# Kernel optimization log

Measured on AMD Instinct MI355X. Metric: run time of the kernel, lower is better.

## Reference

```python
import jax, jax.numpy as jnp
import numpy as np

N_PER = 128   # nodes per graph
G = 256       # graphs in batch
DEG = 4       # out-degree per node
IN = 768
H = 256
R = 4         # num_relations
C = 4         # num classes
RATIO = 0.25
N = G * N_PER
E_G = N_PER * DEG
E = G * E_G
K = int(np.ceil(RATIO * E_G))  # edges kept per graph by sparse_topk


def _build_edges():
    # per graph: edges (i, (i+o) mod n) for o in 1..DEG; offsets < n/2 so the
    # symmetrized edge set has no duplicate pairs (torch.unique is a no-op)
    i = np.arange(N_PER)
    src_l = np.concatenate([i for _ in range(DEG)])
    dst_l = np.concatenate([(i + o) % N_PER for o in range(1, DEG + 1)])
    offs = np.repeat(np.arange(G) * N_PER, E_G)
    src = np.tile(src_l, G) + offs
    dst = np.tile(dst_l, G) + offs
    return jnp.asarray(np.stack([src, dst]), dtype=jnp.int32)


def setup_inputs() -> dict:
    key = jax.random.key(0)
    ks = jax.random.split(key, 20)
    s = 0.02
    inp = {
        'x': jax.random.normal(ks[0], (N, IN), jnp.float32),
        'edge_index': _build_edges(),
        'edge_type': jax.random.randint(ks[1], (E,), 0, R, jnp.int32),
        'y': jax.random.randint(ks[2], (G,), 0, C, jnp.int32),
        # Generator
        'gen_w': jax.random.normal(ks[3], (IN, H), jnp.float32) * s,
        'gen_b': jnp.zeros((H,), jnp.float32),
        'att_w1': jax.random.normal(ks[4], (2 * H, 4 * H), jnp.float32) * s,
        'att_b1': jnp.zeros((4 * H,), jnp.float32),
        'att_w2': jax.random.normal(ks[5], (4 * H, 1), jnp.float32) * s,
        'att_b2': jnp.zeros((1,), jnp.float32),
        # RGCNEncoder
        'in_w': jax.random.normal(ks[6], (IN, H), jnp.float32) * s,
        'in_b': jnp.zeros((H,), jnp.float32),
        'rel_w': jax.random.normal(ks[7], (2, R, H, H), jnp.float32) * s,
        'root_w': jax.random.normal(ks[8], (2, H, H), jnp.float32) * s,
        'conv_b': jnp.zeros((2, H), jnp.float32),
        # classifier head
        'cls_w1': jax.random.normal(ks[9], (2 * H, H), jnp.float32) * s,
        'cls_b1': jnp.zeros((H,), jnp.float32),
        'cls_w2': jax.random.normal(ks[10], (H, C), jnp.float32) * s,
        'cls_b2': jnp.zeros((C,), jnp.float32),
    }
    return inp


def _rgcn_encode(x, ei, et, in_w, in_b, rel_w, root_w, conv_b):
    # linear_in + LeakyReLU
    h = jax.nn.leaky_relu(x @ in_w + in_b)
    src, dst = ei[0], ei[1]
    for l in range(2):  # two RGCNConv layers (dropout is identity in eval)
        out = h @ root_w[l] + conv_b[l]
        for r in range(R):  # per-relation gather-transform-scatter, mean aggr
            m = (et == r)
            xw = h @ rel_w[l, r]                            # [N,H]
            msg = jnp.where(m[:, None], xw[src], 0.0)       # [E,H]
            agg = jax.ops.segment_sum(msg, dst, num_segments=N)
            deg = jax.ops.segment_sum(m.astype(h.dtype), dst, num_segments=N)
            out = out + agg / jnp.maximum(deg, 1.0)[:, None]
        h = out
    ptr = jnp.arange(G) * N_PER  # data.ptr[:-1]: first node of each graph
    return h[ptr]                # [G,H]


def reference(x, edge_index, edge_type, y, gen_w, gen_b, att_w1, att_b1,
              att_w2, att_b2, in_w, in_b, rel_w, root_w, conv_b,
              cls_w1, cls_b1, cls_w2, cls_b2):
    src, dst = edge_index[0], edge_index[1]

    # ----- initial representation on the full graph -----
    initial_rep = _rgcn_encode(x, edge_index, edge_type,
                               in_w, in_b, rel_w, root_w, conv_b)

    # ----- Generator: edge scores -----
    hg = jax.nn.leaky_relu(x @ gen_w + gen_b)
    edge_rep = jnp.concatenate([hg[src], hg[dst]], axis=-1)      # [E,2H]
    score = (jax.nn.relu(edge_rep @ att_w1 + att_b1) @ att_w2 + att_b2)
    score = score.reshape(-1)                                    # [E]

    # ----- split_graph: per-graph top-k (ratio=0.25, descending) -----
    # edges are grouped contiguously per graph with E_G edges each
    sg = score.reshape(G, E_G)
    _, idx = jax.lax.top_k(sg, K)                                # [G,K]
    kept = (idx + (jnp.arange(G) * E_G)[:, None]).reshape(-1)    # global ids

    # ----- graph_sample: keep + symmetrize (unique is a no-op here) -----
    ks_, kd_, kt_ = src[kept], dst[kept], edge_type[kept]
    ei2 = jnp.stack([jnp.concatenate([ks_, kd_]),
                     jnp.concatenate([kd_, ks_])])               # [2, 2*G*K]
    et2 = jnp.concatenate([kt_, kt_])

    learned_rep = _rgcn_encode(x, ei2, et2,
                               in_w, in_b, rel_w, root_w, conv_b)

    # ----- classifier + cross entropy -----
    rep = jnp.concatenate([initial_rep, learned_rep], axis=-1)   # [G,2H]
    logits = jax.nn.leaky_relu(rep @ cls_w1 + cls_b1) @ cls_w2 + cls_b2
    logp = jax.nn.log_softmax(logits, axis=-1)
    loss = -jnp.mean(logp[jnp.arange(G), y])
    return (logits, loss, y)
```

## Files before the change

### kernel.cpp

```cpp
#include <hip/hip_runtime.h>
#include <hip/hip_bf16.h>

typedef __bf16 bf16_t;
typedef __bf16 bf16x8 __attribute__((ext_vector_type(8)));
typedef __bf16 bf16x4 __attribute__((ext_vector_type(4)));
typedef float  f32x4  __attribute__((ext_vector_type(4)));

#define NNODES 32768
#define NPER   128
#define NGRAPH 256
#define NEDGE  131072
#define EPERG  512
#define KKEEP  128
#define M1     5376
#define PLANE1 (M1 * 256)

__global__ void prep_kernel(const float* __restrict__ in_w,
                            const float* __restrict__ gen_w,
                            const float* __restrict__ att_w1,
                            const float* __restrict__ rel_w,
                            const float* __restrict__ root_w,
                            const float* __restrict__ in_b,
                            const float* __restrict__ gen_b,
                            bf16_t* __restrict__ wbf,
                            bf16_t* __restrict__ attT,
                            bf16_t* __restrict__ lw,
                            float*  __restrict__ biasws)
{
  int idx = blockIdx.x * 256 + threadIdx.x;
  if (idx < 393216) {
    int which = idx / 196608, rem = idx % 196608;
    int n = rem / 768, k = rem % 768;
    const float* w = which ? gen_w : in_w;
    wbf[idx] = (bf16_t)w[k * 256 + n];
  } else if (idx < 917504) {
    int i2 = idx - 393216;
    int half = i2 / 262144, rem = i2 % 262144;
    int n = rem / 256, k = rem % 256;
    attT[i2] = (bf16_t)att_w1[(half * 256 + k) * 1024 + n];
  } else if (idx < 1572864) {
    int i3 = idx - 917504;
    int l = i3 / 327680, rem = i3 % 327680;
    int z = rem / 65536, r2 = rem % 65536;
    int n = r2 / 256, k = r2 % 256;
    float v = (z == 0) ? root_w[(l * 256 + k) * 256 + n]
                       : rel_w[((l * 4 + (z - 1)) * 256 + k) * 256 + n];
    lw[i3] = (bf16_t)v;
  } else if (idx < 1573376) {
    int j = idx - 1572864;
    biasws[j] = (j < 256) ? in_b[j] : gen_b[j - 256];
  }
}

__global__ void cast_x_kernel(const float* __restrict__ x, bf16_t* __restrict__ xb)
{
  long i = (long)blockIdx.x * 256 + threadIdx.x;
  const float4* xf = (const float4*)x;
  float4 a = xf[i * 2], b = xf[i * 2 + 1];
  bf16x8 v;
  v[0] = (bf16_t)a.x; v[1] = (bf16_t)a.y; v[2] = (bf16_t)a.z; v[3] = (bf16_t)a.w;
  v[4] = (bf16_t)b.x; v[5] = (bf16_t)b.y; v[6] = (bf16_t)b.z; v[7] = (bf16_t)b.w;
  ((bf16x8*)xb)[i] = v;
}

template<int ACT, bool HAS_BIAS, typename OUT_T>
__global__ __launch_bounds__(512, 1) void gemm_bt2(
    const bf16_t* __restrict__ A, const bf16_t* __restrict__ BT,
    const float* __restrict__ bias, OUT_T* __restrict__ C,
    int M, int K, int colShift, long slabStride)
{
  __shared__ bf16_t sA[8192];
  __shared__ bf16_t sB[16384];
  const int tid = threadIdx.x;
  const int lane = tid & 63, wid = tid >> 6;
  const int wr = wid >> 2, wc = wid & 3;
  const long row0 = (long)blockIdx.x * 128;
  const long n0  = (long)blockIdx.y * 256;

  f32x4 acc[4][4];
  #pragma unroll
  for (int m = 0; m < 4; ++m)
    #pragma unroll
    for (int n = 0; n < 4; ++n)
      #pragma unroll
      for (int j = 0; j < 4; ++j) acc[m][n][j] = 0.f;

  for (int kt = 0; kt < K; kt += 64) {
    #pragma unroll
    for (int p = 0; p < 2; ++p) {
      const int P = p * 8192 + tid * 16;
      const int row = P >> 7;
      const int cch = ((P >> 4) & 7) ^ (row & 7);
      const bf16_t* ga = A + (row0 + row) * (long)K + kt + cch * 8;
      bf16_t* la = sA + p * 4096 + wid * 512;
      __builtin_amdgcn_global_load_lds((__attribute__((address_space(1))) void*)ga,
                                       (__attribute__((address_space(3))) void*)la, 16, 0, 0);
    }
    #pragma unroll
    for (int q = 0; q < 4; ++q) {
      const int P = q * 8192 + tid * 16;
      const int row = P >> 7;
      const int cch = ((P >> 4) & 7) ^ (row & 7);
      const bf16_t* gb = BT + (n0 + row) * (long)K + kt + cch * 8;
      bf16_t* lb = sB + q * 4096 + wid * 512;
      __builtin_amdgcn_global_load_lds((__attribute__((address_space(1))) void*)gb,
                                       (__attribute__((address_space(3))) void*)lb, 16, 0, 0);
    }
    __syncthreads();
    const char* cA = (const char*)sA;
    const char* cB = (const char*)sB;
    #pragma unroll
    for (int kk = 0; kk < 2; ++kk) {
      bf16x8 af[4], bfr[4];
      #pragma unroll
      for (int m = 0; m < 4; ++m) {
        const int row = wr * 64 + m * 16 + (lane & 15);
        const int inb = (((lane >> 4) * 16) + kk * 64) ^ ((row & 7) << 4);
        af[m] = *(const bf16x8*)(cA + row * 128 + inb);
      }
      #pragma unroll
      for (int n = 0; n < 4; ++n) {
        const int row = wc * 64 + n * 16 + (lane & 15);
        const int inb = (((lane >> 4) * 16) + kk * 64) ^ ((row & 7) << 4);
        bfr[n] = *(const bf16x8*)(cB + row * 128 + inb);
      }
      #pragma unroll
      for (int m = 0; m < 4; ++m)
        #pragma unroll
        for (int n = 0; n < 4; ++n)
          acc[m][n] = __builtin_amdgcn_mfma_f32_16x16x32_bf16(af[m], bfr[n], acc[m][n], 0, 0, 0);
    }
    __syncthreads();
  }
  const int ncolsM1 = (1 << colShift) - 1;
  #pragma unroll
  for (int n = 0; n < 4; ++n) {
    const int col = (int)n0 + wc * 64 + n * 16 + (lane & 15);
    const int slab = col >> colShift;
    const int cin = col & ncolsM1;
    float bv = 0.f;
    if (HAS_BIAS) bv = bias[col];
    #pragma unroll
    for (int m = 0; m < 4; ++m) {
      #pragma unroll
      for (int j = 0; j < 4; ++j) {
        const long row = row0 + wr * 64 + m * 16 + (lane >> 4) * 4 + j;
        float v = acc[m][n][j] + bv;
        if (ACT == 1) v = (v > 0.f) ? v : 0.01f * v;
        C[(long)slab * slabStride + (row << colShift) + cin] = (OUT_T)v;
      }
    }
  }
}

__global__ void score_kernel(const bf16_t* __restrict__ Abuf, const bf16_t* __restrict__ Bbuf,
                             const int* __restrict__ src, const int* __restrict__ dst,
                             const float* __restrict__ b1, const float* __restrict__ w2,
                             const float* __restrict__ b2, float* __restrict__ scores)
{
  __shared__ float sb1[1024], sw2[1024];
  for (int i = threadIdx.x; i < 1024; i += 256) { sb1[i] = b1[i]; sw2[i] = w2[i]; }
  __syncthreads();
  const int wid = threadIdx.x >> 6, lane = threadIdx.x & 63;
  const int e = blockIdx.x * 4 + wid;
  const int s = src[e], d = dst[e];
  const bf16x8* ar = (const bf16x8*)(Abuf + (long)s * 1024);
  const bf16x8* br = (const bf16x8*)(Bbuf + (long)d * 1024);
  float acc = 0.f;
  #pragma unroll
  for (int half = 0; half < 2; ++half) {
    bf16x8 av = ar[lane * 2 + half];
    bf16x8 bv = br[lane * 2 + half];
    const int jb = (lane * 2 + half) * 8;
    #pragma unroll
    for (int j = 0; j < 8; ++j) {
      float v = (float)av[j] + (float)bv[j] + sb1[jb + j];
      v = v > 0.f ? v : 0.f;
      acc += v * sw2[jb + j];
    }
  }
  #pragma unroll
  for (int off = 32; off > 0; off >>= 1) acc += __shfl_down(acc, off);
  if (lane == 0) scores[e] = acc + b2[0];
}

__global__ void topk_kernel(const float* __restrict__ scores,
                            const int* __restrict__ src, const int* __restrict__ dst,
                            const int* __restrict__ et,
                            int* __restrict__ ksrc, int* __restrict__ kdst, int* __restrict__ ktyp)
{
  const int g = blockIdx.x;
  __shared__ float sc[512];
  __shared__ int   id[512];
  for (int i = threadIdx.x; i < 512; i += 256) { sc[i] = scores[g * 512 + i]; id[i] = i; }
  for (int k2 = 2; k2 <= 512; k2 <<= 1) {
    for (int j = k2 >> 1; j > 0; j >>= 1) {
      __syncthreads();
      for (int t = threadIdx.x; t < 512; t += 256) {
        const int p = t ^ j;
        if (p > t) {
          float s1 = sc[t], s2 = sc[p];
          int   i1 = id[t], i2 = id[p];
          bool kgt = (s1 < s2) || (s1 == s2 && i1 > i2);
          bool up  = ((t & k2) == 0);
          if (kgt == up) { sc[t] = s2; sc[p] = s1; id[t] = i2; id[p] = i1; }
        }
      }
    }
  }
  __syncthreads();
  if (threadIdx.x < 128) {
    const int e = g * 512 + id[threadIdx.x];
    const int o = g * 128 + threadIdx.x;
    ksrc[o] = src[e]; kdst[o] = dst[e]; ktyp[o] = et[e];
  }
}

__global__ void csr_count(const int* __restrict__ ksrc, const int* __restrict__ kdst,
                          int* __restrict__ counts)
{
  const int i = blockIdx.x * 256 + threadIdx.x;
  if (i >= NGRAPH * KKEEP) return;
  atomicAdd(&counts[kdst[i]], 1);
  atomicAdd(&counts[ksrc[i]], 1);
}

__global__ void csr_offsets(const int* __restrict__ counts, int* __restrict__ offs,
                            int* __restrict__ cursor)
{
  const int g = blockIdx.x, t = threadIdx.x;
  __shared__ int s[128];
  const int mc = counts[g * 128 + t];
  s[t] = mc;
  __syncthreads();
  for (int dd = 1; dd < 128; dd <<= 1) {
    int v = (t >= dd) ? s[t - dd] : 0;
    __syncthreads();
    s[t] += v;
    __syncthreads();
  }
  const int o = g * 256 + (s[t] - mc);
  offs[g * 128 + t] = o;
  cursor[g * 128 + t] = o;
}

__global__ void csr_fill(const int* __restrict__ ksrc, const int* __restrict__ kdst,
                         const int* __restrict__ ktyp, int* __restrict__ cursor,
                         int* __restrict__ nsrc, int* __restrict__ ntyp)
{
  const int i = blockIdx.x * 256 + threadIdx.x;
  if (i >= NGRAPH * KKEEP) return;
  const int s = ksrc[i], d = kdst[i], t = ktyp[i];
  int p = atomicAdd(&cursor[d], 1); nsrc[p] = s; ntyp[p] = t;
  int q = atomicAdd(&cursor[s], 1); nsrc[q] = d; ntyp[q] = t;
}


__global__ void agg_struct_sel(const bf16_t* __restrict__ xw0, const int* __restrict__ et,
                               const float* __restrict__ conv_b, bf16_t* __restrict__ h1g)
{
  const int wid = threadIdx.x >> 6, lane = threadIdx.x & 63;
  const int row = blockIdx.x * 4 + wid;
  const int g = row / 5, slot = row % 5;
  const int d = (slot == 0) ? 0 : (128 - slot);
  const int n = g * 128 + d;
  const int c = lane * 4;
  int rt[4], si[4];
  #pragma unroll
  for (int oo = 0; oo < 4; ++oo) {
    const int i = (d - oo - 1 + 128) & 127;
    rt[oo] = et[g * 512 + oo * 128 + i];
    si[oo] = g * 128 + i;
  }
  const float4 cb = *(const float4*)(conv_b + c);
  bf16x4 rv = *(const bf16x4*)(xw0 + (long)n * 256 + c);
  float acc[4] = { (float)rv[0] + cb.x, (float)rv[1] + cb.y,
                   (float)rv[2] + cb.z, (float)rv[3] + cb.w };
  float s0[4] = {0,0,0,0}, s1[4] = {0,0,0,0}, s2[4] = {0,0,0,0}, s3[4] = {0,0,0,0};
  int d0 = 0, d1 = 0, d2 = 0, d3 = 0;
  #pragma unroll
  for (int oo = 0; oo < 4; ++oo) {
    const int t = rt[oo];
    bf16x4 w = *(const bf16x4*)(xw0 + ((long)(t + 1) * NNODES + si[oo]) * 256 + c);
    if (t == 0)      { d0++; for (int j = 0; j < 4; ++j) s0[j] += (float)w[j]; }
    else if (t == 1) { d1++; for (int j = 0; j < 4; ++j) s1[j] += (float)w[j]; }
    else if (t == 2) { d2++; for (int j = 0; j < 4; ++j) s2[j] += (float)w[j]; }
    else             { d3++; for (int j = 0; j < 4; ++j) s3[j] += (float)w[j]; }
  }
  if (d0) { float r = 1.f / d0; for (int j = 0; j < 4; ++j) acc[j] += s0[j] * r; }
  if (d1) { float r = 1.f / d1; for (int j = 0; j < 4; ++j) acc[j] += s1[j] * r; }
  if (d2) { float r = 1.f / d2; for (int j = 0; j < 4; ++j) acc[j] += s2[j] * r; }
  if (d3) { float r = 1.f / d3; for (int j = 0; j < 4; ++j) acc[j] += s3[j] * r; }
  bf16x4 ov; for (int j = 0; j < 4; ++j) ov[j] = (bf16_t)acc[j];
  *(bf16x4*)(h1g + (long)row * 256 + c) = ov;
}

__global__ void agg_csr_sel(const bf16_t* __restrict__ xw0, const int* __restrict__ offs,
                            const int* __restrict__ cnts, const int* __restrict__ nsrc,
                            const int* __restrict__ ntyp, const float* __restrict__ conv_b,
                            bf16_t* __restrict__ h1g)
{
  const int wid = threadIdx.x >> 6, lane = threadIdx.x & 63;
  const int idx = blockIdx.x * 4 + wid;
  const int g = idx >> 4, slot = idx & 15;
  const int off0 = offs[g * 128], cnt0 = cnts[g * 128];
  if (slot > cnt0) return;
  const int v = (slot == 0) ? g * 128 : nsrc[off0 + slot - 1];
  const int row = 1280 + idx;
  const int offv = offs[v], cntv = cnts[v];
  const int c = lane * 4;
  const float4 cb = *(const float4*)(conv_b + c);
  bf16x4 rv = *(const bf16x4*)(xw0 + (long)v * 256 + c);
  float acc[4] = { (float)rv[0] + cb.x, (float)rv[1] + cb.y,
                   (float)rv[2] + cb.z, (float)rv[3] + cb.w };
  float s0[4] = {0,0,0,0}, s1[4] = {0,0,0,0}, s2[4] = {0,0,0,0}, s3[4] = {0,0,0,0};
  int d0 = 0, d1 = 0, d2 = 0, d3 = 0;
  for (int j = 0; j < cntv; ++j) {
    const int t = ntyp[offv + j];
    const int sv = nsrc[offv + j];
    bf16x4 w = *(const bf16x4*)(xw0 + ((long)(t + 1) * NNODES + sv) * 256 + c);
    if (t == 0)      { d0++; for (int q = 0; q < 4; ++q) s0[q] += (float)w[q]; }
    else if (t == 1) { d1++; for (int q = 0; q < 4; ++q) s1[q] += (float)w[q]; }
    else if (t == 2) { d2++; for (int q = 0; q < 4; ++q) s2[q] += (float)w[q]; }
    else             { d3++; for (int q = 0; q < 4; ++q) s3[q] += (float)w[q]; }
  }
  if (d0) { float r = 1.f / d0; for (int q = 0; q < 4; ++q) acc[q] += s0[q] * r; }
  if (d1) { float r = 1.f / d1; for (int q = 0; q < 4; ++q) acc[q] += s1[q] * r; }
  if (d2) { float r = 1.f / d2; for (int q = 0; q < 4; ++q) acc[q] += s2[q] * r; }
  if (d3) { float r = 1.f / d3; for (int q = 0; q < 4; ++q) acc[q] += s3[q] * r; }
  bf16x4 ov; for (int q = 0; q < 4; ++q) ov[q] = (bf16_t)acc[q];
  *(bf16x4*)(h1g + (long)row * 256 + c) = ov;
}

__global__ void fagg_init(const bf16_t* __restrict__ xw1, const int* __restrict__ et,
                          const float* __restrict__ conv_b1, float* __restrict__ h2I)
{
  const int wid = threadIdx.x >> 6, lane = threadIdx.x & 63;
  const int g = blockIdx.x * 4 + wid;
  const int base = g * 5;
  const int c = lane * 4;
  const float4 cb = *(const float4*)(conv_b1 + c);
  bf16x4 rv = *(const bf16x4*)(xw1 + (long)base * 256 + c);
  float acc[4] = { (float)rv[0] + cb.x, (float)rv[1] + cb.y,
                   (float)rv[2] + cb.z, (float)rv[3] + cb.w };
  float s0[4] = {0,0,0,0}, s1[4] = {0,0,0,0}, s2[4] = {0,0,0,0}, s3[4] = {0,0,0,0};
  int d0 = 0, d1 = 0, d2 = 0, d3 = 0;
  #pragma unroll
  for (int o = 1; o <= 4; ++o) {
    const int t = et[g * 512 + (o - 1) * 128 + (128 - o)];
    bf16x4 w = *(const bf16x4*)(xw1 + ((long)(t + 1) * M1 + base + o) * 256 + c);
    if (t == 0)      { d0++; for (int q = 0; q < 4; ++q) s0[q] += (float)w[q]; }
    else if (t == 1) { d1++; for (int q = 0; q < 4; ++q) s1[q] += (float)w[q]; }
    else if (t == 2) { d2++; for (int q = 0; q < 4; ++q) s2[q] += (float)w[q]; }
    else             { d3++; for (int q = 0; q < 4; ++q) s3[q] += (float)w[q]; }
  }
  if (d0) { float r = 1.f / d0; for (int q = 0; q < 4; ++q) acc[q] += s0[q] * r; }
  if (d1) { float r = 1.f / d1; for (int q = 0; q < 4; ++q) acc[q] += s1[q] * r; }
  if (d2) { float r = 1.f / d2; for (int q = 0; q < 4; ++q) acc[q] += s2[q] * r; }
  if (d3) { float r = 1.f / d3; for (int q = 0; q < 4; ++q) acc[q] += s3[q] * r; }
  *(float4*)(h2I + (long)g * 256 + c) = make_float4(acc[0], acc[1], acc[2], acc[3]);
}

__global__ void fagg_learn(const bf16_t* __restrict__ xw1, const int* __restrict__ offs,
                           const int* __restrict__ cnts, const int* __restrict__ ntyp,
                           const float* __restrict__ conv_b1, float* __restrict__ h2L)
{
  const int wid = threadIdx.x >> 6, lane = threadIdx.x & 63;
  const int g = blockIdx.x * 4 + wid;
  const int base = 1280 + g * 16;
  const int off0 = offs[g * 128], cnt0 = cnts[g * 128];
  const int c = lane * 4;
  const float4 cb = *(const float4*)(conv_b1 + c);
  bf16x4 rv = *(const bf16x4*)(xw1 + (long)base * 256 + c);
  float acc[4] = { (float)rv[0] + cb.x, (float)rv[1] + cb.y,
                   (float)rv[2] + cb.z, (float)rv[3] + cb.w };
  float s0[4] = {0,0,0,0}, s1[4] = {0,0,0,0}, s2[4] = {0,0,0,0}, s3[4] = {0,0,0,0};
  int d0 = 0, d1 = 0, d2 = 0, d3 = 0;
  for (int j = 0; j < cnt0; ++j) {
    const int t = ntyp[off0 + j];
    bf16x4 w = *(const bf16x4*)(xw1 + ((long)(t + 1) * M1 + base + 1 + j) * 256 + c);
    if (t == 0)      { d0++; for (int q = 0; q < 4; ++q) s0[q] += (float)w[q]; }
    else if (t == 1) { d1++; for (int q = 0; q < 4; ++q) s1[q] += (float)w[q]; }
    else if (t == 2) { d2++; for (int q = 0; q < 4; ++q) s2[q] += (float)w[q]; }
    else             { d3++; for (int q = 0; q < 4; ++q) s3[q] += (float)w[q]; }
  }
  if (d0) { float r = 1.f / d0; for (int q = 0; q < 4; ++q) acc[q] += s0[q] * r; }
  if (d1) { float r = 1.f / d1; for (int q = 0; q < 4; ++q) acc[q] += s1[q] * r; }
  if (d2) { float r = 1.f / d2; for (int q = 0; q < 4; ++q) acc[q] += s2[q] * r; }
  if (d3) { float r = 1.f / d3; for (int q = 0; q < 4; ++q) acc[q] += s3[q] * r; }
  *(float4*)(h2L + (long)g * 256 + c) = make_float4(acc[0], acc[1], acc[2], acc[3]);
}

__global__ void classifier_kernel(const float* __restrict__ h2I, const float* __restrict__ h2L,
                                  const float* __restrict__ w1, const float* __restrict__ b1,
                                  const float* __restrict__ w2, const float* __restrict__ b2,
                                  const int* __restrict__ y, float* __restrict__ out,
                                  float* __restrict__ logp)
{
  const int g = blockIdx.x, t = threadIdx.x;
  __shared__ float rep[512];
  __shared__ float hid[256];
  __shared__ float lg[4];
  rep[t] = h2I[g * 256 + t];
  rep[256 + t] = h2L[g * 256 + t];
  __syncthreads();
  float a = b1[t];
  for (int i = 0; i < 512; ++i) a += rep[i] * w1[i * 256 + t];
  hid[t] = a > 0.f ? a : 0.01f * a;
  __syncthreads();
  if (t < 4) {
    float s = b2[t];
    for (int j = 0; j < 256; ++j) s += hid[j] * w2[j * 4 + t];
    lg[t] = s;
    out[g * 4 + t] = s;
  }
  __syncthreads();
  if (t == 0) {
    float m = fmaxf(fmaxf(lg[0], lg[1]), fmaxf(lg[2], lg[3]));
    float se = expf(lg[0] - m) + expf(lg[1] - m) + expf(lg[2] - m) + expf(lg[3] - m);
    logp[g] = lg[y[g]] - (m + logf(se));
  }
}

__global__ void finalize_kernel(const float* __restrict__ logp, const int* __restrict__ y,
                                float* __restrict__ out)
{
  __shared__ float s[256];
  const int t = threadIdx.x;
  s[t] = logp[t];
  __syncthreads();
  for (int d = 128; d > 0; d >>= 1) {
    if (t < d) s[t] += s[t + d];
    __syncthreads();
  }
  if (t == 0) out[1024] = -s[0] / 256.f;
  out[1025 + t] = (float)y[t];
}

extern "C" void kernel_launch(void* const* d_in, const int* in_sizes, int n_in,
                              void* d_out, int out_size, void* d_ws, size_t ws_size,
                              hipStream_t stream)
{
  (void)in_sizes; (void)n_in; (void)out_size; (void)ws_size;
  const float* x      = (const float*)d_in[0];
  const int*   ei     = (const int*)d_in[1];
  const int*   et     = (const int*)d_in[2];
  const int*   y      = (const int*)d_in[3];
  const float* gen_w  = (const float*)d_in[4];
  const float* gen_b  = (const float*)d_in[5];
  const float* att_w1 = (const float*)d_in[6];
  const float* att_b1 = (const float*)d_in[7];
  const float* att_w2 = (const float*)d_in[8];
  const float* att_b2 = (const float*)d_in[9];
  const float* in_w   = (const float*)d_in[10];
  const float* in_b   = (const float*)d_in[11];
  const float* rel_w  = (const float*)d_in[12];
  const float* root_w = (const float*)d_in[13];
  const float* conv_b = (const float*)d_in[14];
  const float* cls_w1 = (const float*)d_in[15];
  const float* cls_b1 = (const float*)d_in[16];
  const float* cls_w2 = (const float*)d_in[17];
  const float* cls_b2 = (const float*)d_in[18];
  const int* src = ei;
  const int* dst = ei + NEDGE;

  char* ws = (char*)d_ws;
  size_t off = 134217728;
  const size_t oBIG = 0;
  auto alloc = [&](size_t bytes) { size_t r = off; off += (bytes + 255) & ~(size_t)255; return r; };
  const size_t oH0  = alloc((size_t)NNODES * 256 * 2);
  const size_t oHG  = alloc((size_t)NNODES * 256 * 2);
  const size_t oH1G = alloc((size_t)M1 * 256 * 2);
  const size_t oXW1 = alloc((size_t)5 * M1 * 256 * 2);
  const size_t oSC  = alloc((size_t)NEDGE * 4);
  const size_t oKS  = alloc((size_t)NGRAPH * KKEEP * 4);
  const size_t oKD  = alloc((size_t)NGRAPH * KKEEP * 4);
  const size_t oKT  = alloc((size_t)NGRAPH * KKEEP * 4);
  const size_t oCNT = alloc((size_t)NNODES * 4);
  const size_t oOFF = alloc((size_t)NNODES * 4);
  const size_t oCUR = alloc((size_t)NNODES * 4);
  const size_t oNS  = alloc((size_t)2 * NGRAPH * KKEEP * 4);
  const size_t oNT  = alloc((size_t)2 * NGRAPH * KKEEP * 4);
  const size_t oWBF = alloc((size_t)2 * 256 * 768 * 2);
  const size_t oATT = alloc((size_t)2 * 1024 * 256 * 2);
  const size_t oLW  = alloc((size_t)2 * 5 * 256 * 256 * 2);
  const size_t oBIA = alloc(512 * 4);
  const size_t oH2I = alloc((size_t)NGRAPH * 256 * 4);
  const size_t oH2L = alloc((size_t)NGRAPH * 256 * 4);
  const size_t oLP  = alloc((size_t)NGRAPH * 4);

  bf16_t* xbf  = (bf16_t*)(ws + oBIG);
  bf16_t* AB   = (bf16_t*)(ws + oBIG);
  bf16_t* xw0  = (bf16_t*)(ws + oBIG);
  bf16_t* h0   = (bf16_t*)(ws + oH0);
  bf16_t* hg   = (bf16_t*)(ws + oHG);
  bf16_t* h1g  = (bf16_t*)(ws + oH1G);
  bf16_t* xw1  = (bf16_t*)(ws + oXW1);
  bf16_t* wbf  = (bf16_t*)(ws + oWBF);
  bf16_t* attT = (bf16_t*)(ws + oATT);
  bf16_t* lw   = (bf16_t*)(ws + oLW);
  float*  bias = (float*)(ws + oBIA);

  prep_kernel<<<6146, 256, 0, stream>>>(in_w, gen_w, att_w1, rel_w, root_w, in_b, gen_b,
                                        wbf, attT, lw, bias);
  cast_x_kernel<<<12288, 256, 0, stream>>>(x, xbf);

  gemm_bt2<1, true, bf16_t><<<dim3(256, 2), 512, 0, stream>>>(
      xbf, wbf, bias, h0, NNODES, 768, 8, 8388608L);

  gemm_bt2<0, false, bf16_t><<<dim3(256, 8), 512, 0, stream>>>(
      hg, attT, nullptr, AB, NNODES, 256, 10, 33554432L);
  score_kernel<<<32768, 256, 0, stream>>>(AB, AB + 33554432L, src, dst, att_b1, att_w2,
                                          att_b2, (float*)(ws + oSC));

  topk_kernel<<<NGRAPH, 256, 0, stream>>>((const float*)(ws + oSC), src, dst, et,
                                          (int*)(ws + oKS), (int*)(ws + oKD), (int*)(ws + oKT));
  hipMemsetAsync(ws + oCNT, 0, (size_t)NNODES * 4, stream);
  csr_count<<<128, 256, 0, stream>>>((const int*)(ws + oKS), (const int*)(ws + oKD), (int*)(ws + oCNT));
  csr_offsets<<<NGRAPH, 128, 0, stream>>>((const int*)(ws + oCNT), (int*)(ws + oOFF), (int*)(ws + oCUR));
  csr_fill<<<128, 256, 0, stream>>>((const int*)(ws + oKS), (const int*)(ws + oKD),
                                    (const int*)(ws + oKT), (int*)(ws + oCUR),
                                    (int*)(ws + oNS), (int*)(ws + oNT));

  gemm_bt2<0, false, bf16_t><<<dim3(256, 5), 512, 0, stream>>>(
      h0, lw, nullptr, xw0, NNODES, 256, 8, 8388608L);

  agg_struct_sel<<<320, 256, 0, stream>>>(xw0, et, conv_b, h1g);
  agg_csr_sel<<<1024, 256, 0, stream>>>(xw0, (const int*)(ws + oOFF), (const int*)(ws + oCNT),
                                        (const int*)(ws + oNS), (const int*)(ws + oNT),
                                        conv_b, h1g);

  gemm_bt2<0, false, bf16_t><<<dim3(42, 5), 512, 0, stream>>>(
      h1g, lw + 5 * 65536, nullptr, xw1, M1, 256, 8, (long)PLANE1);

  fagg_init<<<64, 256, 0, stream>>>(xw1, et, conv_b + 256, (float*)(ws + oH2I));
  fagg_learn<<<64, 256, 0, stream>>>(xw1, (const int*)(ws + oOFF), (const int*)(ws + oCNT),
                                     (const int*)(ws + oNT), conv_b + 256, (float*)(ws + oH2L));

  classifier_kernel<<<NGRAPH, 256, 0, stream>>>((const float*)(ws + oH2I), (const float*)(ws + oH2L),
                                                cls_w1, cls_b1, cls_w2, cls_b2, y,
                                                (float*)d_out, (float*)(ws + oLP));
  finalize_kernel<<<1, 256, 0, stream>>>((const float*)(ws + oLP), y, (float*)d_out);
}
```

Baseline: 494.4 us.

## Fuse fp32-to-bf16 cast into first GEMM and stage epilogue through LDS

Drops the separate cast_x kernel and converts fp32 x to bf16 inside the first GEMM's A-tile load, writing the swizzled result into shared memory with ordinary loads and stores. That removes one full read/write pass over x in bf16. The GEMM epilogue now stages each 16-row group in shared memory and writes 16-byte vectors to global memory instead of scattered 2-byte stores. Launch bounds also rise to allow 4 blocks per CU. The cast path gives up async global_load_lds for register-routed loads, and the epilogue adds extra barriers.

```diff
diff --git a/kernel.cpp b/kernel.cpp
--- a/kernel.cpp
+++ b/kernel.cpp
@@ -14,6 +14,7 @@
 #define KKEEP  128
 #define M1     5376
 #define PLANE1 (M1 * 256)
+#define EPS    264
 
 __global__ void prep_kernel(const float* __restrict__ in_w,
                             const float* __restrict__ gen_w,
@@ -52,21 +53,10 @@
   }
 }
 
-__global__ void cast_x_kernel(const float* __restrict__ x, bf16_t* __restrict__ xb)
-{
-  long i = (long)blockIdx.x * 256 + threadIdx.x;
-  const float4* xf = (const float4*)x;
-  float4 a = xf[i * 2], b = xf[i * 2 + 1];
-  bf16x8 v;
-  v[0] = (bf16_t)a.x; v[1] = (bf16_t)a.y; v[2] = (bf16_t)a.z; v[3] = (bf16_t)a.w;
-  v[4] = (bf16_t)b.x; v[5] = (bf16_t)b.y; v[6] = (bf16_t)b.z; v[7] = (bf16_t)b.w;
-  ((bf16x8*)xb)[i] = v;
-}
-
-template<int ACT, bool HAS_BIAS, typename OUT_T>
-__global__ __launch_bounds__(512, 1) void gemm_bt2(
-    const bf16_t* __restrict__ A, const bf16_t* __restrict__ BT,
-    const float* __restrict__ bias, OUT_T* __restrict__ C,
+template<int ACT, bool HAS_BIAS, bool CAST_A>
+__global__ __launch_bounds__(512, 4) void gemm_bt2(
+    const void* __restrict__ Araw, const bf16_t* __restrict__ BT,
+    const float* __restrict__ bias, bf16_t* __restrict__ C,
     int M, int K, int colShift, long slabStride)
 {
   __shared__ bf16_t sA[8192];
@@ -86,15 +76,33 @@
       for (int j = 0; j < 4; ++j) acc[m][n][j] = 0.f;
 
   for (int kt = 0; kt < K; kt += 64) {
-    #pragma unroll
-    for (int p = 0; p < 2; ++p) {
-      const int P = p * 8192 + tid * 16;
-      const int row = P >> 7;
-      const int cch = ((P >> 4) & 7) ^ (row & 7);
-      const bf16_t* ga = A + (row0 + row) * (long)K + kt + cch * 8;
-      bf16_t* la = sA + p * 4096 + wid * 512;
-      __builtin_amdgcn_global_load_lds((__attribute__((address_space(1))) void*)ga,
-                                       (__attribute__((address_space(3))) void*)la, 16, 0, 0);
+    if constexpr (CAST_A) {
+      const float* Af = (const float*)Araw;
+      #pragma unroll
+      for (int p = 0; p < 2; ++p) {
+        const int idx = p * 4096 + tid * 8;
+        const int row = idx >> 6;
+        const int k8  = idx & 63;
+        const float4* g = (const float4*)(Af + (row0 + row) * (long)K + kt + k8);
+        float4 a = g[0], b = g[1];
+        bf16x8 v;
+        v[0]=(bf16_t)a.x; v[1]=(bf16_t)a.y; v[2]=(bf16_t)a.z; v[3]=(bf16_t)a.w;
+        v[4]=(bf16_t)b.x; v[5]=(bf16_t)b.y; v[6]=(bf16_t)b.z; v[7]=(bf16_t)b.w;
+        const int chunk = (k8 >> 3) ^ (row & 7);
+        *(bf16x8*)((char*)sA + row * 128 + chunk * 16) = v;
+      }
+    } else {
+      const bf16_t* A = (const bf16_t*)Araw;
+      #pragma unroll
+      for (int p = 0; p < 2; ++p) {
+        const int P = p * 8192 + tid * 16;
+        const int row = P >> 7;
+        const int cch = ((P >> 4) & 7) ^ (row & 7);
+        const bf16_t* ga = A + (row0 + row) * (long)K + kt + cch * 8;
+        bf16_t* la = sA + p * 4096 + wid * 512;
+        __builtin_amdgcn_global_load_lds((__attribute__((address_space(1))) void*)ga,
+                                         (__attribute__((address_space(3))) void*)la, 16, 0, 0);
+      }
     }
     #pragma unroll
     for (int q = 0; q < 4; ++q) {
@@ -116,7 +124,7 @@
       for (int m = 0; m < 4; ++m) {
         const int row = wr * 64 + m * 16 + (lane & 15);
         const int inb = (((lane >> 4) * 16) + kk * 64) ^ ((row & 7) << 4);
-        af[m] = *(const bf16x8*)(cA + row * 128 + inb);
+        af[m] = *(const bf16x8*)(cA + (row & 127) * 128 + inb);
       }
       #pragma unroll
       for (int n = 0; n < 4; ++n) {
@@ -132,24 +140,38 @@
     }
     __syncthreads();
   }
+
   const int ncolsM1 = (1 << colShift) - 1;
-  #pragma unroll
-  for (int n = 0; n < 4; ++n) {
-    const int col = (int)n0 + wc * 64 + n * 16 + (lane & 15);
-    const int slab = col >> colShift;
-    const int cin = col & ncolsM1;
-    float bv = 0.f;
-    if (HAS_BIAS) bv = bias[col];
+  bf16_t* tb = sB;
+  #pragma unroll
+  for (int mg = 0; mg < 4; ++mg) {
     #pragma unroll
-    for (int m = 0; m < 4; ++m) {
+    for (int n = 0; n < 4; ++n) {
+      const int col = wc * 64 + n * 16 + (lane & 15);
+      float bv = 0.f;
+      if (HAS_BIAS) bv = bias[(int)n0 + col];
       #pragma unroll
       for (int j = 0; j < 4; ++j) {
-        const long row = row0 + wr * 64 + m * 16 + (lane >> 4) * 4 + j;
-        float v = acc[m][n][j] + bv;
+        const int lrow = wr * 16 + (lane >> 4) * 4 + j;
+        float v = acc[mg][n][j] + bv;
         if (ACT == 1) v = (v > 0.f) ? v : 0.01f * v;
-        C[(long)slab * slabStride + (row << colShift) + cin] = (OUT_T)v;
+        tb[lrow * EPS + col] = (bf16_t)v;
       }
     }
+    __syncthreads();
+    #pragma unroll
+    for (int p = 0; p < 2; ++p) {
+      const int idx = p * 512 + tid;
+      const int lrow = idx >> 5;
+      const int c8 = (idx & 31) * 8;
+      bf16x8 v = *(const bf16x8*)(tb + lrow * EPS + c8);
+      const long row = row0 + (lrow >> 4) * 64 + mg * 16 + (lrow & 15);
+      const int gcol = (int)n0 + c8;
+      const int slab = gcol >> colShift;
+      const int cin = gcol & ncolsM1;
+      *(bf16x8*)(C + (long)slab * slabStride + (row << colShift) + cin) = v;
+    }
+    __syncthreads();
   }
 }
 
@@ -489,7 +511,6 @@
   const size_t oH2L = alloc((size_t)NGRAPH * 256 * 4);
   const size_t oLP  = alloc((size_t)NGRAPH * 4);
 
-  bf16_t* xbf  = (bf16_t*)(ws + oBIG);
   bf16_t* AB   = (bf16_t*)(ws + oBIG);
   bf16_t* xw0  = (bf16_t*)(ws + oBIG);
   bf16_t* h0   = (bf16_t*)(ws + oH0);
@@ -503,13 +524,12 @@
 
   prep_kernel<<<6146, 256, 0, stream>>>(in_w, gen_w, att_w1, rel_w, root_w, in_b, gen_b,
                                         wbf, attT, lw, bias);
-  cast_x_kernel<<<12288, 256, 0, stream>>>(x, xbf);
-
-  gemm_bt2<1, true, bf16_t><<<dim3(256, 2), 512, 0, stream>>>(
-      xbf, wbf, bias, h0, NNODES, 768, 8, 8388608L);
-
-  gemm_bt2<0, false, bf16_t><<<dim3(256, 8), 512, 0, stream>>>(
-      hg, attT, nullptr, AB, NNODES, 256, 10, 33554432L);
+
+  gemm_bt2<1, true, true><<<dim3(256, 2), 512, 0, stream>>>(
+      (const void*)x, wbf, bias, h0, NNODES, 768, 8, 8388608L);
+
+  gemm_bt2<0, false, false><<<dim3(256, 8), 512, 0, stream>>>(
+      (const void*)hg, attT, nullptr, AB, NNODES, 256, 10, 33554432L);
   score_kernel<<<32768, 256, 0, stream>>>(AB, AB + 33554432L, src, dst, att_b1, att_w2,
                                           att_b2, (float*)(ws + oSC));
 
@@ -522,16 +542,16 @@
                                     (const int*)(ws + oKT), (int*)(ws + oCUR),
                                     (int*)(ws + oNS), (int*)(ws + oNT));
 
-  gemm_bt2<0, false, bf16_t><<<dim3(256, 5), 512, 0, stream>>>(
-      h0, lw, nullptr, xw0, NNODES, 256, 8, 8388608L);
+  gemm_bt2<0, false, false><<<dim3(256, 5), 512, 0, stream>>>(
+      (const void*)h0, lw, nullptr, xw0, NNODES, 256, 8, 8388608L);
 
   agg_struct_sel<<<320, 256, 0, stream>>>(xw0, et, conv_b, h1g);
   agg_csr_sel<<<1024, 256, 0, stream>>>(xw0, (const int*)(ws + oOFF), (const int*)(ws + oCNT),
                                         (const int*)(ws + oNS), (const int*)(ws + oNT),
                                         conv_b, h1g);
 
-  gemm_bt2<0, false, bf16_t><<<dim3(42, 5), 512, 0, stream>>>(
-      h1g, lw + 5 * 65536, nullptr, xw1, M1, 256, 8, (long)PLANE1);
+  gemm_bt2<0, false, false><<<dim3(42, 5), 512, 0, stream>>>(
+      (const void*)h1g, lw + 5 * 65536, nullptr, xw1, M1, 256, 8, (long)PLANE1);
 
   fagg_init<<<64, 256, 0, stream>>>(xw1, et, conv_b + 256, (float*)(ws + oH2I));
   fagg_learn<<<64, 256, 0, stream>>>(xw1, (const int*)(ws + oOFF), (const int*)(ws + oCNT),
```

New measurement: 441.9 us. 10.6% less time.
